# Optimization experiments

Hardware: AMD Instinct MI355X
Metric: run time of the kernel (lower is better)

Reference implementation:

```python
import jax, jax.numpy as jnp
import numpy as np

NUM_CLASSES = 19
RMI_RADIUS = 3
POOL_SIZE = 3
POOL_STRIDE = 3
IGNORE_INDEX = 255
LOSS_WEIGHT = 1.0


def _avg_pool_nchw(x, k, s):
    # torch F.avg_pool2d with padding=k//2, count_include_pad=True
    p = k // 2
    summed = jax.lax.reduce_window(
        x, 0.0, jax.lax.add,
        window_dimensions=(1, 1, k, k),
        window_strides=(1, 1, s, s),
        padding=[(0, 0), (0, 0), (p, p), (p, p)])
    return summed / float(k * k)


def _map_get_pairs(labels, probs, radius):
    h, w = labels.shape[2], labels.shape[3]
    nh, nw = h - radius + 1, w - radius + 1
    la = jnp.stack([labels[:, :, y:y + nh, x:x + nw]
                    for y in range(radius) for x in range(radius)], axis=2)
    pr = jnp.stack([probs[:, :, y:y + nh, x:x + nw]
                    for y in range(radius) for x in range(radius)], axis=2)
    return la, pr  # (N, C, r*r, nh, nw)


def _log_det_by_cholesky(mat):
    chol = jnp.linalg.cholesky(mat)
    diag = jnp.diagonal(chol, axis1=-2, axis2=-1)
    return 2.0 * jnp.sum(jnp.log(diag + 1e-8), axis=-1)


def _rmi_lower_bound(labels_4d, probs_4d):
    labels_4d = _avg_pool_nchw(labels_4d, POOL_SIZE, POOL_STRIDE)
    probs_4d = _avg_pool_nchw(probs_4d, POOL_SIZE, POOL_STRIDE)
    la, pr = _map_get_pairs(labels_4d, probs_4d, RMI_RADIUS)
    N, C, D = la.shape[:3]
    la = la.reshape(N, C, D, -1)   # (N, C, D, M)
    pr = pr.reshape(N, C, D, -1)
    M = la.shape[-1]
    la = la - la.mean(axis=-1, keepdims=True)
    pr = pr - pr.mean(axis=-1, keepdims=True)
    la_cov = jnp.einsum('ncdm,ncem->ncde', la, la) / M
    pr_cov = jnp.einsum('ncdm,ncem->ncde', pr, pr) / M
    pr_la_cov = jnp.einsum('ncdm,ncem->ncde', pr, la) / M
    eye = jnp.eye(D, dtype=la_cov.dtype)
    la_cov_inv = jnp.linalg.inv(la_cov + eye * 1e-5)
    appro_var = pr_cov - jnp.einsum('ncde,ncef,ncgf->ncdg',
                                    pr_la_cov, la_cov_inv, pr_la_cov)
    appro_var = appro_var + eye * 1e-6
    rmi_per_class = 0.5 * _log_det_by_cholesky(appro_var)  # (N, C)
    rmi_per_class = rmi_per_class.mean(axis=0)             # (C,)
    return jnp.sum(rmi_per_class) / NUM_CLASSES


def setup_inputs() -> dict:
    key = jax.random.key(0)
    k1, k2 = jax.random.split(key)
    cls_score = jax.random.normal(k1, (4, 19, 512, 512), dtype=jnp.float32)
    label = jax.random.randint(k2, (4, 512, 512), 0, NUM_CLASSES, dtype=jnp.int64)
    return {"cls_score": cls_score, "label": label}


def reference(cls_score, label):
    probs = jax.nn.softmax(cls_score.astype(jnp.float32), axis=1)
    valid = (label >= 0) & (label < NUM_CLASSES) & (label != IGNORE_INDEX)
    lbl = jnp.where(valid, label, 0)
    onehot = jax.nn.one_hot(lbl, NUM_CLASSES, dtype=jnp.float32)
    onehot = jnp.transpose(onehot, (0, 3, 1, 2))  # (N, C, H, W)
    vmask = valid[:, None, :, :].astype(jnp.float32)
    onehot = onehot * vmask
    probs = probs * vmask
    loss = _rmi_lower_bound(onehot, probs)
    return LOSS_WEIGHT * loss
```

## Files before the change

### kernel.cpp

```cpp
#include <hip/hip_runtime.h>
#include <math.h>

#define NBATCH 4
#define NCLS   19
#define HWDIM  512
#define HW     (512 * 512)
#define PH     171
#define PHP    176
#define PP2A   (171 * 176)
#define NHW    169
#define MM     (169 * 169)
#define NBAND  11
#define NSTRIP 43

typedef float f4 __attribute__((ext_vector_type(4)));
typedef float f2 __attribute__((ext_vector_type(2)));

__global__ __launch_bounds__(512) void stage1_pool(
    const float* __restrict__ cls, const int* __restrict__ label,
    float* __restrict__ P, float* __restrict__ L) {
  int n  = blockIdx.x / PH;
  int ph = blockIdx.x - n * PH;
  int col = threadIdx.x;

  float accP[NCLS], accL[NCLS];
#pragma unroll
  for (int c = 0; c < NCLS; ++c) { accP[c] = 0.f; accL[c] = 0.f; }

#pragma unroll
  for (int i = 0; i < 3; ++i) {
    int r = 3 * ph - 1 + i;
    if (r < 0 || r >= HWDIM) continue;
    int lb = label[((size_t)n * HWDIM + r) * HWDIM + col];
    const float* base = cls + (size_t)n * NCLS * HW + (size_t)r * HWDIM + col;
    float v[NCLS];
    float mx = -INFINITY;
#pragma unroll
    for (int c = 0; c < NCLS; ++c) {
      v[c] = base[(size_t)c * HW];
      mx = fmaxf(mx, v[c]);
    }
    float se = 0.f;
#pragma unroll
    for (int c = 0; c < NCLS; ++c) {
      v[c] = expf(v[c] - mx);
      se += v[c];
    }
    if (lb >= 0 && lb < NCLS) {
      float inv = 1.f / se;
#pragma unroll
      for (int c = 0; c < NCLS; ++c) {
        accP[c] += v[c] * inv;
        accL[c] += (lb == c) ? 1.f : 0.f;
      }
    }
  }

  __shared__ float xbP[4][516];
  __shared__ float xbL[4][516];
  const float inv9 = 1.f / 9.f;
#pragma unroll
  for (int c0 = 0; c0 < NCLS; c0 += 4) {
    int nc_round = (NCLS - c0) < 4 ? (NCLS - c0) : 4;
#pragma unroll
    for (int cc = 0; cc < 4; ++cc) {
      if (cc < nc_round) {
        xbP[cc][1 + col] = accP[(c0 + cc) < NCLS ? (c0 + cc) : 0];
        xbL[cc][1 + col] = accL[(c0 + cc) < NCLS ? (c0 + cc) : 0];
        if (col == 0) { xbP[cc][0] = 0.f; xbL[cc][0] = 0.f; }
      }
    }
    __syncthreads();
    if (col < PH) {
      int pw = col;
#pragma unroll
      for (int cc = 0; cc < 4; ++cc) {
        if (cc < nc_round) {
          int c = c0 + cc;
          float sP = xbP[cc][3 * pw] + xbP[cc][3 * pw + 1] + xbP[cc][3 * pw + 2];
          float sL = xbL[cc][3 * pw] + xbL[cc][3 * pw + 1] + xbL[cc][3 * pw + 2];
          size_t o = ((size_t)(n * NCLS + c)) * PP2A + (size_t)ph * PHP + pw;
          P[o] = sP * inv9;
          L[o] = sL * inv9;
        }
      }
    } else if (col < PHP) {
#pragma unroll
      for (int cc = 0; cc < 4; ++cc) {
        if (cc < nc_round) {
          int c = c0 + cc;
          size_t o = ((size_t)(n * NCLS + c)) * PP2A + (size_t)ph * PHP + col;
          P[o] = 0.f;
          L[o] = 0.f;
        }
      }
    }
    __syncthreads();
  }
}

template <int PART>
__device__ __forceinline__ void mom_body(
    const float* __restrict__ Pp, const float* __restrict__ Lp,
    float* __restrict__ covp, int nc, float* red) {
  constexpr int NA  = (PART == 0) ? 63 : (PART == 1 ? 45 : 81);
  constexpr int OFF = (PART == 0) ? 0  : (PART == 1 ? 63 : 108);

  float acc[NA];
#pragma unroll
  for (int k = 0; k < NA; ++k) acc[k] = 0.f;

  int tid = threadIdx.x;
  if (tid < NSTRIP * NBAND) {
    int b  = tid / NSTRIP;
    int s  = tid - b * NSTRIP;
    int x0 = 4 * s;
    int y0 = (NHW * b) / NBAND;
    int y1 = (NHW * (b + 1)) / NBAND;

    float wp[18], wl[18];
#pragma unroll
    for (int r = 0; r < 3; ++r) {
      const float* rp = Pp + (y0 + r) * PHP + x0;
      *(f4*)&wp[r * 6]     = *(const f4*)rp;
      *(f2*)&wp[r * 6 + 4] = *(const f2*)(rp + 4);
      if (PART != 1) {
        const float* rl = Lp + (y0 + r) * PHP + x0;
        *(f4*)&wl[r * 6]     = *(const f4*)rl;
        *(f2*)&wl[r * 6 + 4] = *(const f2*)(rl + 4);
      }
    }

    for (int y = y0; y < y1; ++y) {
      int yn = (y + 3 <= PH - 1) ? (y + 3) : (PH - 1);
      const float* rp = Pp + yn * PHP + x0;
      f4 tp4 = *(const f4*)rp;
      f2 tp2 = *(const f2*)(rp + 4);
      f4 tl4; f2 tl2;
      if (PART != 1) {
        const float* rl = Lp + yn * PHP + x0;
        tl4 = *(const f4*)rl;
        tl2 = *(const f2*)(rl + 4);
      }
#pragma unroll
      for (int p = 0; p < 4; ++p) {
        if (x0 + p < NHW) {
          if (PART == 0) {
#pragma unroll
            for (int dy = 0; dy < 3; ++dy)
#pragma unroll
              for (int dx = 0; dx < 3; ++dx) {
                int d = dy * 3 + dx;
                acc[d]     += wl[dy * 6 + p + dx];
                acc[9 + d] += wp[dy * 6 + p + dx];
              }
            int k = 18;
#pragma unroll
            for (int d = 0; d < 9; ++d)
#pragma unroll
              for (int e = d; e < 9; ++e) {
                acc[k] += wl[(d / 3) * 6 + p + (d % 3)] *
                          wl[(e / 3) * 6 + p + (e % 3)];
                ++k;
              }
          } else if (PART == 1) {
            int k = 0;
#pragma unroll
            for (int d = 0; d < 9; ++d)
#pragma unroll
              for (int e = d; e < 9; ++e) {
                acc[k] += wp[(d / 3) * 6 + p + (d % 3)] *
                          wp[(e / 3) * 6 + p + (e % 3)];
                ++k;
              }
          } else {
#pragma unroll
            for (int d = 0; d < 9; ++d)
#pragma unroll
              for (int e = 0; e < 9; ++e)
                acc[d * 9 + e] += wp[(d / 3) * 6 + p + (d % 3)] *
                                  wl[(e / 3) * 6 + p + (e % 3)];
          }
        }
      }
#pragma unroll
      for (int t = 0; t < 12; ++t) {
        wp[t] = wp[t + 6];
        if (PART != 1) wl[t] = wl[t + 6];
      }
      *(f4*)&wp[12] = tp4;
      *(f2*)&wp[16] = tp2;
      if (PART != 1) {
        *(f4*)&wl[12] = tl4;
        *(f2*)&wl[16] = tl2;
      }
    }
  }

  int lane = threadIdx.x & 63;
  int wid  = threadIdx.x >> 6;
#pragma unroll
  for (int k = 0; k < NA; ++k) {
    float v = acc[k];
#pragma unroll
    for (int o = 32; o > 0; o >>= 1) v += __shfl_down(v, o, 64);
    if (lane == 0) red[wid * NA + k] = v;
  }
  __syncthreads();
  if (threadIdx.x < NA) {
    float sm = 0.f;
#pragma unroll
    for (int w = 0; w < 8; ++w) sm += red[w * NA + threadIdx.x];
    covp[(size_t)nc * 192 + OFF + threadIdx.x] = sm;
  }
}

__global__ __launch_bounds__(512) void stage2_mom(
    const float* __restrict__ P, const float* __restrict__ L,
    float* __restrict__ covp) {
  __shared__ float red[8 * 81];
  int nc = blockIdx.x;
  const float* Pp = P + (size_t)nc * PP2A;
  const float* Lp = L + (size_t)nc * PP2A;
  if (blockIdx.y == 0)      mom_body<0>(Pp, Lp, covp, nc, red);
  else if (blockIdx.y == 1) mom_body<1>(Pp, Lp, covp, nc, red);
  else                      mom_body<2>(Pp, Lp, covp, nc, red);
}

__global__ __launch_bounds__(64) void stage3_rmi(float* __restrict__ covp) {
  int nc  = blockIdx.x;
  int tid = threadIdx.x;
  const float* s = covp + (size_t)nc * 192;
  __shared__ double lc[81], pc[81], plc[81], mla[9], mpr[9];
  const double Minv = 1.0 / (double)MM;

  if (tid < 9)       mla[tid]     = (double)s[tid] * Minv;
  else if (tid < 18) mpr[tid - 9] = (double)s[tid] * Minv;
  __syncthreads();

  for (int e = tid; e < 81; e += 64) {
    int r = e / 9, c = e - 9 * (e / 9);
    int lo = r < c ? r : c, hi = r < c ? c : r;
    int k = lo * 9 - lo * (lo - 1) / 2 + (hi - lo);
    double a = (double)s[18 + k] * Minv - mla[r] * mla[c];
    if (r == c) a += 1e-5;
    lc[e] = a;
    pc[e] = (double)s[63 + k] * Minv - mpr[r] * mpr[c];
    plc[e] = (double)s[108 + e] * Minv - mpr[r] * mla[c];
  }
  __syncthreads();

  for (int j = 0; j < 9; ++j) {
    if (tid == 0) lc[j * 9 + j] = sqrt(lc[j * 9 + j]);
    __syncthreads();
    if (tid > j && tid < 9) lc[tid * 9 + j] /= lc[j * 9 + j];
    __syncthreads();
    if (tid > j && tid < 9) {
      double lij = lc[tid * 9 + j];
      for (int k = j + 1; k <= tid; ++k) lc[tid * 9 + k] -= lij * lc[k * 9 + j];
    }
    __syncthreads();
  }

  if (tid < 9) {
    int d = tid;
    for (int j = 0; j < 9; ++j) {
      double t = plc[d * 9 + j];
      for (int k = 0; k < j; ++k) t -= plc[d * 9 + k] * lc[j * 9 + k];
      plc[d * 9 + j] = t / lc[j * 9 + j];
    }
  }
  __syncthreads();

  for (int e = tid; e < 81; e += 64) {
    int r = e / 9, c = e - 9 * (e / 9);
    double a = pc[e];
    for (int f = 0; f < 9; ++f) a -= plc[r * 9 + f] * plc[c * 9 + f];
    if (r == c) a += 1e-6;
    pc[e] = a;
  }
  __syncthreads();

  for (int j = 0; j < 9; ++j) {
    if (tid == 0) pc[j * 9 + j] = sqrt(pc[j * 9 + j]);
    __syncthreads();
    if (tid > j && tid < 9) pc[tid * 9 + j] /= pc[j * 9 + j];
    __syncthreads();
    if (tid > j && tid < 9) {
      double lij = pc[tid * 9 + j];
      for (int k = j + 1; k <= tid; ++k) pc[tid * 9 + k] -= lij * pc[k * 9 + j];
    }
    __syncthreads();
  }

  if (tid == 0) {
    double sl = 0.0;
    for (int j = 0; j < 9; ++j) sl += log(pc[j * 9 + j] + 1e-8);
    *(double*)(covp + (size_t)nc * 192 + 190) = sl;
  }
}

__global__ __launch_bounds__(64) void stage4_reduce(
    const float* __restrict__ covp, float* __restrict__ out) {
  int tid = threadIdx.x;
  double v = 0.0;
  if (tid < NBATCH * NCLS)
    v = *(const double*)(covp + (size_t)tid * 192 + 190);
  if (tid + 64 < NBATCH * NCLS)
    v += *(const double*)(covp + (size_t)(tid + 64) * 192 + 190);
#pragma unroll
  for (int o = 32; o > 0; o >>= 1) v += __shfl_down(v, o, 64);
  if (tid == 0) out[0] = (float)(v / (double)(NBATCH * NCLS));
}

extern "C" void kernel_launch(void* const* d_in, const int* in_sizes, int n_in,
                              void* d_out, int out_size, void* d_ws, size_t ws_size,
                              hipStream_t stream) {
  const float* cls  = (const float*)d_in[0];
  const int* label  = (const int*)d_in[1];
  float* out = (float*)d_out;

  float* P    = (float*)d_ws;
  float* L    = P + (size_t)NBATCH * NCLS * PP2A;
  float* covp = L + (size_t)NBATCH * NCLS * PP2A;

  stage1_pool<<<NBATCH * PH, 512, 0, stream>>>(cls, label, P, L);
  dim3 g2(NBATCH * NCLS, 3, 1);
  stage2_mom<<<g2, 512, 0, stream>>>(P, L, covp);
  stage3_rmi<<<NBATCH * NCLS, 64, 0, stream>>>(covp);
  stage4_reduce<<<1, 64, 0, stream>>>(covp, out);
}
```

Baseline: 76.56 us.

## Vectorize moment accumulation with packed float2 and rebalance stage2 work split

Rewrites the stage-2 moment kernel so each thread accumulates two adjacent output positions in float2 vectors, aiming to use packed FMA instructions. Label and prob self-moments are split evenly into two modes (mean+self products each), and the cross term uses a different strip/band layout with a separate tail-thread path for the last column. The reduction now shuffles only to 8 lanes and sums 64 partials from shared memory. This cuts the wave-level shuffle reductions, at the cost of higher register pressure and a larger shared-memory footprint.

```diff
diff --git a/kernel.cpp b/kernel.cpp
--- a/kernel.cpp
+++ b/kernel.cpp
@@ -10,11 +10,9 @@
 #define PP2A   (171 * 176)
 #define NHW    169
 #define MM     (169 * 169)
-#define NBAND  11
-#define NSTRIP 43
-
-typedef float f4 __attribute__((ext_vector_type(4)));
-typedef float f2 __attribute__((ext_vector_type(2)));
+
+typedef float f4  __attribute__((ext_vector_type(4)));
+typedef float f2v __attribute__((ext_vector_type(2)));
 
 __global__ __launch_bounds__(512) void stage1_pool(
     const float* __restrict__ cls, const int* __restrict__ label,
@@ -99,132 +97,210 @@
   }
 }
 
-template <int PART>
-__device__ __forceinline__ void mom_body(
-    const float* __restrict__ Pp, const float* __restrict__ Lp,
-    float* __restrict__ covp, int nc, float* red) {
-  constexpr int NA  = (PART == 0) ? 63 : (PART == 1 ? 45 : 81);
-  constexpr int OFF = (PART == 0) ? 0  : (PART == 1 ? 63 : 108);
-
-  float acc[NA];
-#pragma unroll
-  for (int k = 0; k < NA; ++k) acc[k] = 0.f;
-
+template <int MODE, int NA>
+__device__ __forceinline__ void epilogue(const f2v (&acc2)[NA], float* red,
+                                         float* __restrict__ covp, int nc) {
+  int lane = threadIdx.x & 63;
+  int wid  = threadIdx.x >> 6;
+#pragma unroll
+  for (int k = 0; k < NA; ++k) {
+    float v = acc2[k].x + acc2[k].y;
+    v += __shfl_down(v, 32, 64);
+    v += __shfl_down(v, 16, 64);
+    v += __shfl_down(v, 8, 64);
+    if (lane < 8) red[(wid * 8 + lane) * 84 + k] = v;
+  }
+  __syncthreads();
   int tid = threadIdx.x;
-  if (tid < NSTRIP * NBAND) {
-    int b  = tid / NSTRIP;
-    int s  = tid - b * NSTRIP;
+  if (tid < NA) {
+    float sm = 0.f;
+#pragma unroll
+    for (int w = 0; w < 64; ++w) sm += red[w * 84 + tid];
+    int off;
+    if (MODE == 0)      off = (tid < 9) ? tid : 18 + (tid - 9);
+    else if (MODE == 1) off = (tid < 9) ? 9 + tid : 63 + (tid - 9);
+    else                off = 108 + tid;
+    covp[(size_t)nc * 192 + off] = sm;
+  }
+}
+
+template <int MODE>
+__device__ __forceinline__ void mom_self(const float* __restrict__ X,
+                                         float* __restrict__ covp, int nc,
+                                         float* red) {
+  f2v acc2[54];
+#pragma unroll
+  for (int k = 0; k < 54; ++k) acc2[k] = (f2v){0.f, 0.f};
+
+  int tid = threadIdx.x;
+  if (tid < 462) {
+    int b = tid / 42, s = tid - b * 42;
     int x0 = 4 * s;
-    int y0 = (NHW * b) / NBAND;
-    int y1 = (NHW * (b + 1)) / NBAND;
-
-    float wp[18], wl[18];
+    int y0 = (NHW * b) / 11;
+    int y1 = (NHW * (b + 1)) / 11;
+
+    f2v w[3][5];
 #pragma unroll
     for (int r = 0; r < 3; ++r) {
-      const float* rp = Pp + (y0 + r) * PHP + x0;
-      *(f4*)&wp[r * 6]     = *(const f4*)rp;
-      *(f2*)&wp[r * 6 + 4] = *(const f2*)(rp + 4);
-      if (PART != 1) {
-        const float* rl = Lp + (y0 + r) * PHP + x0;
-        *(f4*)&wl[r * 6]     = *(const f4*)rl;
-        *(f2*)&wl[r * 6 + 4] = *(const f2*)(rl + 4);
-      }
+      f4  a  = *(const f4*)(X + (y0 + r) * PHP + x0);
+      f2v bb = *(const f2v*)(X + (y0 + r) * PHP + x0 + 4);
+      w[r][0] = (f2v){a.x, a.y}; w[r][1] = (f2v){a.y, a.z};
+      w[r][2] = (f2v){a.z, a.w}; w[r][3] = (f2v){a.w, bb.x};
+      w[r][4] = bb;
     }
 
     for (int y = y0; y < y1; ++y) {
       int yn = (y + 3 <= PH - 1) ? (y + 3) : (PH - 1);
-      const float* rp = Pp + yn * PHP + x0;
-      f4 tp4 = *(const f4*)rp;
-      f2 tp2 = *(const f2*)(rp + 4);
-      f4 tl4; f2 tl2;
-      if (PART != 1) {
-        const float* rl = Lp + yn * PHP + x0;
-        tl4 = *(const f4*)rl;
-        tl2 = *(const f2*)(rl + 4);
-      }
-#pragma unroll
-      for (int p = 0; p < 4; ++p) {
-        if (x0 + p < NHW) {
-          if (PART == 0) {
-#pragma unroll
-            for (int dy = 0; dy < 3; ++dy)
-#pragma unroll
-              for (int dx = 0; dx < 3; ++dx) {
-                int d = dy * 3 + dx;
-                acc[d]     += wl[dy * 6 + p + dx];
-                acc[9 + d] += wp[dy * 6 + p + dx];
-              }
-            int k = 18;
-#pragma unroll
-            for (int d = 0; d < 9; ++d)
-#pragma unroll
-              for (int e = d; e < 9; ++e) {
-                acc[k] += wl[(d / 3) * 6 + p + (d % 3)] *
-                          wl[(e / 3) * 6 + p + (e % 3)];
-                ++k;
-              }
-          } else if (PART == 1) {
-            int k = 0;
-#pragma unroll
-            for (int d = 0; d < 9; ++d)
-#pragma unroll
-              for (int e = d; e < 9; ++e) {
-                acc[k] += wp[(d / 3) * 6 + p + (d % 3)] *
-                          wp[(e / 3) * 6 + p + (e % 3)];
-                ++k;
-              }
-          } else {
-#pragma unroll
-            for (int d = 0; d < 9; ++d)
-#pragma unroll
-              for (int e = 0; e < 9; ++e)
-                acc[d * 9 + e] += wp[(d / 3) * 6 + p + (d % 3)] *
-                                  wl[(e / 3) * 6 + p + (e % 3)];
+      f4  a  = *(const f4*)(X + yn * PHP + x0);
+      f2v bb = *(const f2v*)(X + yn * PHP + x0 + 4);
+
+#pragma unroll
+      for (int d = 0; d < 9; ++d) {
+        acc2[d] += w[d / 3][d % 3];
+        acc2[d] += w[d / 3][(d % 3) + 2];
+      }
+      {
+        int k = 9;
+#pragma unroll
+        for (int d = 0; d < 9; ++d)
+#pragma unroll
+          for (int e = d; e < 9; ++e) {
+            acc2[k] += w[d / 3][d % 3] * w[e / 3][e % 3];
+            acc2[k] += w[d / 3][(d % 3) + 2] * w[e / 3][(e % 3) + 2];
+            ++k;
           }
-        }
-      }
-#pragma unroll
-      for (int t = 0; t < 12; ++t) {
-        wp[t] = wp[t + 6];
-        if (PART != 1) wl[t] = wl[t + 6];
-      }
-      *(f4*)&wp[12] = tp4;
-      *(f2*)&wp[16] = tp2;
-      if (PART != 1) {
-        *(f4*)&wl[12] = tl4;
-        *(f2*)&wl[16] = tl2;
-      }
-    }
-  }
-
-  int lane = threadIdx.x & 63;
-  int wid  = threadIdx.x >> 6;
-#pragma unroll
-  for (int k = 0; k < NA; ++k) {
-    float v = acc[k];
-#pragma unroll
-    for (int o = 32; o > 0; o >>= 1) v += __shfl_down(v, o, 64);
-    if (lane == 0) red[wid * NA + k] = v;
-  }
-  __syncthreads();
-  if (threadIdx.x < NA) {
-    float sm = 0.f;
-#pragma unroll
-    for (int w = 0; w < 8; ++w) sm += red[w * NA + threadIdx.x];
-    covp[(size_t)nc * 192 + OFF + threadIdx.x] = sm;
-  }
+      }
+#pragma unroll
+      for (int j = 0; j < 5; ++j) { w[0][j] = w[1][j]; w[1][j] = w[2][j]; }
+      w[2][0] = (f2v){a.x, a.y}; w[2][1] = (f2v){a.y, a.z};
+      w[2][2] = (f2v){a.z, a.w}; w[2][3] = (f2v){a.w, bb.x};
+      w[2][4] = bb;
+    }
+  } else if (tid < 473) {
+    int b  = tid - 462;
+    int y0 = (NHW * b) / 11;
+    int y1 = (NHW * (b + 1)) / 11;
+    float t[3][3];
+#pragma unroll
+    for (int r = 0; r < 3; ++r)
+#pragma unroll
+      for (int c = 0; c < 3; ++c) t[r][c] = X[(y0 + r) * PHP + 168 + c];
+    for (int y = y0; y < y1; ++y) {
+      int yn = (y + 3 <= PH - 1) ? (y + 3) : (PH - 1);
+      float n0 = X[yn * PHP + 168], n1 = X[yn * PHP + 169],
+            n2 = X[yn * PHP + 170];
+#pragma unroll
+      for (int d = 0; d < 9; ++d) acc2[d].x += t[d / 3][d % 3];
+      {
+        int k = 9;
+#pragma unroll
+        for (int d = 0; d < 9; ++d)
+#pragma unroll
+          for (int e = d; e < 9; ++e) {
+            acc2[k].x += t[d / 3][d % 3] * t[e / 3][e % 3];
+            ++k;
+          }
+      }
+#pragma unroll
+      for (int c = 0; c < 3; ++c) { t[0][c] = t[1][c]; t[1][c] = t[2][c]; }
+      t[2][0] = n0; t[2][1] = n1; t[2][2] = n2;
+    }
+  }
+  epilogue<MODE, 54>(acc2, red, covp, nc);
+}
+
+__device__ __forceinline__ void mom_cross(const float* __restrict__ Pp,
+                                          const float* __restrict__ Lp,
+                                          float* __restrict__ covp, int nc,
+                                          float* red) {
+  f2v acc2[81];
+#pragma unroll
+  for (int k = 0; k < 81; ++k) acc2[k] = (f2v){0.f, 0.f};
+
+  int tid = threadIdx.x;
+  if (tid < 504) {
+    int b = tid / 84, s = tid - b * 84;
+    int x0 = 2 * s;
+    int y0 = (NHW * b) / 6;
+    int y1 = (NHW * (b + 1)) / 6;
+
+    f2v wp[3][3], wl[3][3];
+#pragma unroll
+    for (int r = 0; r < 3; ++r) {
+      f2v p01 = *(const f2v*)(Pp + (y0 + r) * PHP + x0);
+      f2v p23 = *(const f2v*)(Pp + (y0 + r) * PHP + x0 + 2);
+      wp[r][0] = p01; wp[r][1] = (f2v){p01.y, p23.x}; wp[r][2] = p23;
+      f2v l01 = *(const f2v*)(Lp + (y0 + r) * PHP + x0);
+      f2v l23 = *(const f2v*)(Lp + (y0 + r) * PHP + x0 + 2);
+      wl[r][0] = l01; wl[r][1] = (f2v){l01.y, l23.x}; wl[r][2] = l23;
+    }
+
+    for (int y = y0; y < y1; ++y) {
+      int yn = (y + 3 <= PH - 1) ? (y + 3) : (PH - 1);
+      f2v p01 = *(const f2v*)(Pp + yn * PHP + x0);
+      f2v p23 = *(const f2v*)(Pp + yn * PHP + x0 + 2);
+      f2v l01 = *(const f2v*)(Lp + yn * PHP + x0);
+      f2v l23 = *(const f2v*)(Lp + yn * PHP + x0 + 2);
+
+#pragma unroll
+      for (int d = 0; d < 9; ++d)
+#pragma unroll
+        for (int e = 0; e < 9; ++e)
+          acc2[d * 9 + e] += wp[d / 3][d % 3] * wl[e / 3][e % 3];
+
+#pragma unroll
+      for (int j = 0; j < 3; ++j) {
+        wp[0][j] = wp[1][j]; wp[1][j] = wp[2][j];
+        wl[0][j] = wl[1][j]; wl[1][j] = wl[2][j];
+      }
+      wp[2][0] = p01; wp[2][1] = (f2v){p01.y, p23.x}; wp[2][2] = p23;
+      wl[2][0] = l01; wl[2][1] = (f2v){l01.y, l23.x}; wl[2][2] = l23;
+    }
+  } else if (tid < 510) {
+    int b  = tid - 504;
+    int y0 = (NHW * b) / 6;
+    int y1 = (NHW * (b + 1)) / 6;
+    float tp[3][3], tl[3][3];
+#pragma unroll
+    for (int r = 0; r < 3; ++r)
+#pragma unroll
+      for (int c = 0; c < 3; ++c) {
+        tp[r][c] = Pp[(y0 + r) * PHP + 168 + c];
+        tl[r][c] = Lp[(y0 + r) * PHP + 168 + c];
+      }
+    for (int y = y0; y < y1; ++y) {
+      int yn = (y + 3 <= PH - 1) ? (y + 3) : (PH - 1);
+      float np0 = Pp[yn * PHP + 168], np1 = Pp[yn * PHP + 169],
+            np2 = Pp[yn * PHP + 170];
+      float nl0 = Lp[yn * PHP + 168], nl1 = Lp[yn * PHP + 169],
+            nl2 = Lp[yn * PHP + 170];
+#pragma unroll
+      for (int d = 0; d < 9; ++d)
+#pragma unroll
+        for (int e = 0; e < 9; ++e)
+          acc2[d * 9 + e].x += tp[d / 3][d % 3] * tl[e / 3][e % 3];
+#pragma unroll
+      for (int c = 0; c < 3; ++c) {
+        tp[0][c] = tp[1][c]; tp[1][c] = tp[2][c];
+        tl[0][c] = tl[1][c]; tl[1][c] = tl[2][c];
+      }
+      tp[2][0] = np0; tp[2][1] = np1; tp[2][2] = np2;
+      tl[2][0] = nl0; tl[2][1] = nl1; tl[2][2] = nl2;
+    }
+  }
+  epilogue<2, 81>(acc2, red, covp, nc);
 }
 
 __global__ __launch_bounds__(512) void stage2_mom(
     const float* __restrict__ P, const float* __restrict__ L,
     float* __restrict__ covp) {
-  __shared__ float red[8 * 81];
+  __shared__ float red[64 * 84];
   int nc = blockIdx.x;
   const float* Pp = P + (size_t)nc * PP2A;
   const float* Lp = L + (size_t)nc * PP2A;
-  if (blockIdx.y == 0)      mom_body<0>(Pp, Lp, covp, nc, red);
-  else if (blockIdx.y == 1) mom_body<1>(Pp, Lp, covp, nc, red);
-  else                      mom_body<2>(Pp, Lp, covp, nc, red);
+  if (blockIdx.y == 0)      mom_self<0>(Lp, covp, nc, red);
+  else if (blockIdx.y == 1) mom_self<1>(Pp, covp, nc, red);
+  else                      mom_cross(Pp, Lp, covp, nc, red);
 }
 
 __global__ __launch_bounds__(64) void stage3_rmi(float* __restrict__ covp) {
```

Result: no change. 76.29 us (-0.4%).
